# Performance work log

Hardware: AMD Instinct MI355X
Metric: run time of the kernel (lower is better)

The kernel has to match this reference:

```python
import jax, jax.numpy as jnp
import numpy as np

BS, TPD, D = 16384, 4, 128
G, M = 4, 4096


def setup_inputs() -> dict:
    key = jax.random.key(0)
    k1, k2 = jax.random.split(key)
    return {
        "x": jax.random.normal(k1, (BS, TPD, D), dtype=jnp.float32),
        "embeddings": jax.random.normal(k2, (G, M, D), dtype=jnp.float32),
        "count": jnp.zeros((G, M), dtype=jnp.float32),
    }


def reference(x, embeddings, count):
    bs, tpd, d = x.shape
    g, m, _ = embeddings.shape
    # (BS, TPD, D) -> (N, G, D) -> (G, N, D), N = BS*TPD/G
    xg = x.reshape(-1, g, d).transpose(1, 0, 2)
    # squared euclidean distances (argmin identical to cdist argmin)
    x2 = jnp.sum(xg * xg, axis=-1)[:, :, None]            # (G, N, 1)
    e2 = jnp.sum(embeddings * embeddings, axis=-1)[:, None, :]  # (G, 1, M)
    dist = x2 + e2 - 2.0 * jnp.einsum('gnd,gmd->gnm', xg, embeddings)  # (G, N, M)
    indices = jnp.argmin(dist, axis=-1)                   # (G, N) int
    # usage-count scatter add (buffer update in torch forward)
    new_count = count.at[jnp.arange(g)[:, None], indices].add(1.0)
    # gather quantized embeddings: (G, N, D)
    x_quant = embeddings[jnp.arange(g)[:, None], indices]
    x_quant = x_quant.transpose(1, 0, 2).reshape(bs, tpd, d)
    ind_out = indices.transpose(1, 0).reshape(bs, tpd)
    return (x_quant, ind_out, new_count)
```

## Files before the change

### kernel.cpp

```cpp
#include <hip/hip_runtime.h>

#define G 4
#define M 4096
#define D 128
#define NQ 16384
#define NROWS 65536
#define OFF_IND 8388608
#define OFF_CNT (OFF_IND + NROWS)
#define DELTA 0.02f

typedef unsigned int u32;
typedef unsigned short u16;
typedef __attribute__((ext_vector_type(8))) short bf16x8;
typedef __attribute__((ext_vector_type(4))) float f32x4;

__device__ __forceinline__ u16 f2bf(float f) {
    u32 u = __float_as_uint(f);
    return (u16)((u + 0x7FFFu + ((u >> 16) & 1u)) >> 16);
}
__device__ __forceinline__ float bf2f(u16 b) { return __uint_as_float((u32)b << 16); }

union bfpack { bf16x8 v; u32 u[4]; };


__global__ __launch_bounds__(256) void prep_emb_e2(const float* __restrict__ emb,
                                                   u32* __restrict__ efrag,
                                                   float* __restrict__ e2f) {
    const int tid = threadIdx.x, lane = tid & 63;
    const int c = blockIdx.x * 4 + (tid >> 6);
    const int ks = c & 3, mt = (c >> 2) & 255, g = c >> 10;
    const int m = mt * 16 + (lane & 15);
    const int k = ks * 32 + (lane >> 4) * 8;
    const float* src = emb + ((size_t)g * M + m) * D + k;
    const float4 a = *(const float4*)src;
    const float4 b = *(const float4*)(src + 4);
    const float v[8] = {a.x, a.y, a.z, a.w, b.x, b.y, b.z, b.w};
    float ss = 0.f;
#pragma unroll
    for (int i = 0; i < 8; ++i) ss = fmaf(v[i], v[i], ss);
    u32 hi[4], lo[4];
#pragma unroll
    for (int i = 0; i < 4; ++i) {
        const float v0 = v[2 * i], v1 = v[2 * i + 1];
        const u16 h0 = f2bf(v0), h1 = f2bf(v1);
        const u16 l0 = f2bf(v0 - bf2f(h0)), l1 = f2bf(v1 - bf2f(h1));
        hi[i] = (u32)h0 | ((u32)h1 << 16);
        lo[i] = (u32)l0 | ((u32)l1 << 16);
    }
    const u32 base = (u32)(g * 256 + mt) * 2048 + (u32)(ks * 2) * 256 + lane * 4;
    *(uint4*)(efrag + base)       = make_uint4(hi[0], hi[1], hi[2], hi[3]);
    *(uint4*)(efrag + base + 256) = make_uint4(lo[0], lo[1], lo[2], lo[3]);
    ss += __shfl_xor(ss, 16, 64);
    ss += __shfl_xor(ss, 32, 64);
    if (lane < 16) atomicAdd(&e2f[g * M + m], ss);
}

__global__ __launch_bounds__(256) void vq_mfma2(const float* __restrict__ x,
                                                const u32* __restrict__ efrag,
                                                const float* __restrict__ e2f,
                                                float* __restrict__ pb1,
                                                float* __restrict__ pb2,
                                                int* __restrict__ pi1) {
    __shared__ float e2s[2048];
    __shared__ u32 ebuf[2][2048];

    const int tid = threadIdx.x, w = tid >> 6, lane = tid & 63;
    const int combo = blockIdx.x & 7;
    const int g = combo >> 1, half = combo & 1;
    const int qb = blockIdx.x >> 3;

    const float* e2g = e2f + (size_t)g * M + half * 2048;
    for (int i = tid; i < 512; i += 256) ((float4*)e2s)[i] = ((const float4*)e2g)[i];

    const int qt0 = qb * 8 + w * 2;
    bf16x8 xf[2][4][2];
#pragma unroll
    for (int f = 0; f < 2; ++f) {
        const int n = (qt0 + f) * 16 + (lane & 15);
#pragma unroll
        for (int ks = 0; ks < 4; ++ks) {
            const int k = ks * 32 + (lane >> 4) * 8;
            const float* src = x + ((size_t)n * 4 + g) * D + k;
            const float4 a = *(const float4*)src;
            const float4 b = *(const float4*)(src + 4);
            const float v[8] = {a.x, a.y, a.z, a.w, b.x, b.y, b.z, b.w};
            bfpack ph, pl;
#pragma unroll
            for (int i = 0; i < 4; ++i) {
                const float v0 = -2.0f * v[2 * i], v1 = -2.0f * v[2 * i + 1];
                const u16 h0 = f2bf(v0), h1 = f2bf(v1);
                const u16 l0 = f2bf(v0 - bf2f(h0)), l1 = f2bf(v1 - bf2f(h1));
                ph.u[i] = (u32)h0 | ((u32)h1 << 16);
                pl.u[i] = (u32)l0 | ((u32)l1 << 16);
            }
            xf[f][ks][0] = ph.v;
            xf[f][ks][1] = pl.v;
        }
    }

    float b1[8], b2[8];
    int i1[8];
#pragma unroll
    for (int s = 0; s < 8; ++s) { b1[s] = 3.4e38f; b2[s] = 3.4e38f; i1[s] = 0; }

    const uint4* eg = (const uint4*)(efrag + (size_t)(g * 256 + half * 128) * 2048);
    {
        const uint4 s0 = eg[tid], s1 = eg[256 + tid];
        ((uint4*)ebuf[0])[tid] = s0;
        ((uint4*)ebuf[0])[256 + tid] = s1;
    }
    __syncthreads();

    int cur = 0;
    const int mb0 = half * 2048;
    for (int mc = 0; mc < 128; ++mc) {
        uint4 s0, s1;
        const bool pf = (mc + 1 < 128);
        if (pf) {
            const uint4* src = eg + (size_t)(mc + 1) * 512;
            s0 = src[tid];
            s1 = src[256 + tid];
        }
        const bf16x8* bp = (const bf16x8*)ebuf[cur];
        bf16x8 bh[4], bl[4];
#pragma unroll
        for (int ks = 0; ks < 4; ++ks) {
            bh[ks] = bp[(ks * 2 + 0) * 64 + lane];
            bl[ks] = bp[(ks * 2 + 1) * 64 + lane];
        }
        const int mcol = mb0 + mc * 16 + (lane & 15);
        const float e2c = e2s[mc * 16 + (lane & 15)];
        const f32x4 init = {e2c, e2c, e2c, e2c};
        f32x4 acc0, acc1;
        acc0 = __builtin_amdgcn_mfma_f32_16x16x32_bf16(xf[0][0][1], bh[0], init, 0, 0, 0);
        acc1 = __builtin_amdgcn_mfma_f32_16x16x32_bf16(xf[1][0][1], bh[0], init, 0, 0, 0);
#pragma unroll
        for (int ks = 1; ks < 4; ++ks) {
            acc0 = __builtin_amdgcn_mfma_f32_16x16x32_bf16(xf[0][ks][1], bh[ks], acc0, 0, 0, 0);
            acc1 = __builtin_amdgcn_mfma_f32_16x16x32_bf16(xf[1][ks][1], bh[ks], acc1, 0, 0, 0);
        }
#pragma unroll
        for (int ks = 0; ks < 4; ++ks) {
            acc0 = __builtin_amdgcn_mfma_f32_16x16x32_bf16(xf[0][ks][0], bl[ks], acc0, 0, 0, 0);
            acc1 = __builtin_amdgcn_mfma_f32_16x16x32_bf16(xf[1][ks][0], bl[ks], acc1, 0, 0, 0);
        }
#pragma unroll
        for (int ks = 0; ks < 4; ++ks) {
            acc0 = __builtin_amdgcn_mfma_f32_16x16x32_bf16(xf[0][ks][0], bh[ks], acc0, 0, 0, 0);
            acc1 = __builtin_amdgcn_mfma_f32_16x16x32_bf16(xf[1][ks][0], bh[ks], acc1, 0, 0, 0);
        }
#pragma unroll
        for (int r = 0; r < 4; ++r) {
            const float s0v = acc0[r];
            b2[r] = fminf(b2[r], fmaxf(b1[r], s0v));
            i1[r] = (s0v < b1[r]) ? mcol : i1[r];
            b1[r] = fminf(b1[r], s0v);
            const float s1v = acc1[r];
            b2[r + 4] = fminf(b2[r + 4], fmaxf(b1[r + 4], s1v));
            i1[r + 4] = (s1v < b1[r + 4]) ? mcol : i1[r + 4];
            b1[r + 4] = fminf(b1[r + 4], s1v);
        }
        if (pf) {
            uint4* dst = (uint4*)ebuf[cur ^ 1];
            dst[tid] = s0;
            dst[256 + tid] = s1;
        }
        __syncthreads();
        cur ^= 1;
    }

#pragma unroll
    for (int s = 0; s < 8; ++s) {
        float v1 = b1[s], v2 = b2[s];
        int j1 = i1[s];
#pragma unroll
        for (int off = 1; off < 16; off <<= 1) {
            const float o1 = __shfl_xor(v1, off, 64);
            const int   oj = __shfl_xor(j1, off, 64);
            const float o2 = __shfl_xor(v2, off, 64);
            v2 = fminf(fminf(v2, o2), fmaxf(v1, o1));
            if (o1 < v1 || (o1 == v1 && oj < j1)) { v1 = o1; j1 = oj; }
        }
        if ((lane & 15) == 0) {
            const int n = (qt0 + (s >> 2)) * 16 + (lane >> 4) * 4 + (s & 3);
            const int pidx = ((((g << 14) | n)) << 1) | half;
            pb1[pidx] = v1;
            pb2[pidx] = v2;
            pi1[pidx] = j1;
        }
    }
}

__global__ __launch_bounds__(256) void merge_kernel(const float* __restrict__ pb1,
                                                    const float* __restrict__ pb2,
                                                    const int* __restrict__ pi1,
                                                    float* __restrict__ out,
                                                    int* __restrict__ flagcnt,
                                                    int* __restrict__ flaglist) {
    const int t = blockIdx.x * 256 + threadIdx.x;
    const float v1a = pb1[2 * t], v1b = pb1[2 * t + 1];
    const float v2a = pb2[2 * t], v2b = pb2[2 * t + 1];
    const int   ia = pi1[2 * t],  ib = pi1[2 * t + 1];
    const float v1 = fminf(v1a, v1b);
    const int   i  = (v1b < v1a) ? ib : ia;
    const float v2 = fminf(fminf(v2a, v2b), fmaxf(v1a, v1b));
    const int g = t >> 14, n = t & 16383;
    if (v2 - v1 > DELTA) {
        out[(size_t)OFF_IND + (size_t)n * 4 + g] = (float)i;
        atomicAdd(out + OFF_CNT + (size_t)g * M + i, 1.0f);
    } else {
        const int pos = atomicAdd(flagcnt, 1);
        flaglist[pos] = t;
    }
}

__global__ __launch_bounds__(256) void recheck(const float* __restrict__ x,
                                               const float* __restrict__ emb,
                                               const int* __restrict__ flagcnt,
                                               const int* __restrict__ flaglist,
                                               float* __restrict__ out) {
    __shared__ float xs[D];
    __shared__ double wv[4];
    __shared__ int wi[4];
    const int tid = threadIdx.x;
    int nf = *flagcnt;
    if (nf > NROWS) nf = NROWS;
    for (int it = blockIdx.x; it < nf; it += gridDim.x) {
        const int qid = flaglist[it];
        const int g = qid >> 14, n = qid & 16383;
        __syncthreads();
        if (tid < 32) ((float4*)xs)[tid] = ((const float4*)(x + ((size_t)n * 4 + g) * D))[tid];
        __syncthreads();
        double best = 1e300;
        int bi = 0;
        for (int j = 0; j < 16; ++j) {
            const int m = tid + j * 256;
            const float* e = emb + ((size_t)g * M + m) * D;
            double dot = 0.0, ee = 0.0;
            for (int k = 0; k < D; k += 4) {
                const float4 ev = *(const float4*)(e + k);
                const double e0 = ev.x, e1 = ev.y, e2v = ev.z, e3 = ev.w;
                dot = fma((double)xs[k + 0], e0, dot);
                dot = fma((double)xs[k + 1], e1, dot);
                dot = fma((double)xs[k + 2], e2v, dot);
                dot = fma((double)xs[k + 3], e3, dot);
                ee = fma(e0, e0, ee); ee = fma(e1, e1, ee);
                ee = fma(e2v, e2v, ee); ee = fma(e3, e3, ee);
            }
            const double s = ee - 2.0 * dot;
            if (s < best) { best = s; bi = m; }
        }
        for (int off = 1; off < 64; off <<= 1) {
            const double ob = __shfl_xor(best, off, 64);
            const int oi = __shfl_xor(bi, off, 64);
            if (ob < best || (ob == best && oi < bi)) { best = ob; bi = oi; }
        }
        if ((tid & 63) == 0) { wv[tid >> 6] = best; wi[tid >> 6] = bi; }
        __syncthreads();
        if (tid == 0) {
            double bv = wv[0];
            int bj = wi[0];
            for (int u = 1; u < 4; ++u)
                if (wv[u] < bv || (wv[u] == bv && wi[u] < bj)) { bv = wv[u]; bj = wi[u]; }
            out[(size_t)OFF_IND + (size_t)n * 4 + g] = (float)bj;
            atomicAdd(out + OFF_CNT + (size_t)g * M + bj, 1.0f);
        }
    }
}

__global__ __launch_bounds__(256) void gather_kernel(const float* __restrict__ emb,
                                                     const float* __restrict__ indf,
                                                     float* __restrict__ xq) {
    const int rid = blockIdx.x * 8 + (threadIdx.x >> 5);
    const int lane = threadIdx.x & 31;
    const int g = rid & 3;
    const int m = (int)indf[rid];
    const float4 v = ((const float4*)(emb + ((size_t)g * M + m) * D))[lane];
    ((float4*)(xq + (size_t)rid * D))[lane] = v;
}


#define QT 64
#define MT 128
#define KT 32
#define XPAD 132
#define EPAD 36

__global__ __launch_bounds__(256) void e2d_kernel(const float* __restrict__ emb,
                                                  double* __restrict__ e2) {
    int row = blockIdx.x * 4 + (threadIdx.x >> 6);
    int lane = threadIdx.x & 63;
    const float2 v = ((const float2*)(emb + (size_t)row * D))[lane];
    double s = (double)v.x * (double)v.x + (double)v.y * (double)v.y;
#pragma unroll
    for (int off = 1; off < 64; off <<= 1) s += __shfl_xor(s, off, 64);
    if (lane == 0) e2[row] = s;
}

__global__ __launch_bounds__(256) void argmin_kernel(const float* __restrict__ x,
                                                     const float* __restrict__ emb,
                                                     const double* __restrict__ e2,
                                                     float* __restrict__ out) {
    __shared__ float xs[QT][XPAD];
    __shared__ float es[MT][EPAD];
    const int g = blockIdx.x >> 8;
    const int n0 = (blockIdx.x & 255) * QT;
    const int tid = threadIdx.x;
    const int tm = tid & 15;
    const int tq = tid >> 4;
#pragma unroll
    for (int it = 0; it < 8; ++it) {
        int idx = it * 256 + tid;
        int r = idx >> 5, c2 = idx & 31;
        const float4 v = ((const float4*)(x + ((size_t)((n0 + r) * 4 + g)) * D))[c2];
        *(float4*)&xs[r][c2 * 4] = v;
    }
    double best[4];
    int bm[4];
#pragma unroll
    for (int qi = 0; qi < 4; ++qi) { best[qi] = 1e300; bm[qi] = 0; }
    const double* e2g = e2 + (size_t)g * M;
    const float* eg = emb + (size_t)g * M * D;
    for (int mc = 0; mc < M / MT; ++mc) {
        const int m0 = mc * MT;
        double acc[4][8];
#pragma unroll
        for (int qi = 0; qi < 4; ++qi)
#pragma unroll
            for (int mi = 0; mi < 8; ++mi) acc[qi][mi] = 0.0;
        for (int kc = 0; kc < D / KT; ++kc) {
            __syncthreads();
#pragma unroll
            for (int it = 0; it < 4; ++it) {
                int idx = it * 256 + tid;
                int r = idx >> 3, c2 = idx & 7;
                const float4 v = ((const float4*)(eg + (size_t)(m0 + r) * D + kc * KT))[c2];
                *(float4*)&es[r][c2 * 4] = v;
            }
            __syncthreads();
#pragma unroll
            for (int kk = 0; kk < KT; kk += 4) {
                double xv[4][4];
#pragma unroll
                for (int qi = 0; qi < 4; ++qi) {
                    const float4 v = *(const float4*)&xs[tq + 16 * qi][kc * KT + kk];
                    xv[qi][0] = v.x; xv[qi][1] = v.y; xv[qi][2] = v.z; xv[qi][3] = v.w;
                }
#pragma unroll
                for (int mi = 0; mi < 8; ++mi) {
                    const float4 v = *(const float4*)&es[tm + 16 * mi][kk];
                    const double e0 = v.x, e1 = v.y, e2v = v.z, e3 = v.w;
#pragma unroll
                    for (int qi = 0; qi < 4; ++qi) {
                        acc[qi][mi] = fma(xv[qi][0], e0, acc[qi][mi]);
                        acc[qi][mi] = fma(xv[qi][1], e1, acc[qi][mi]);
                        acc[qi][mi] = fma(xv[qi][2], e2v, acc[qi][mi]);
                        acc[qi][mi] = fma(xv[qi][3], e3, acc[qi][mi]);
                    }
                }
            }
        }
#pragma unroll
        for (int mi = 0; mi < 8; ++mi) {
            const int m = m0 + tm + 16 * mi;
            const double e2m = e2g[m];
#pragma unroll
            for (int qi = 0; qi < 4; ++qi) {
                const double s = e2m - 2.0 * acc[qi][mi];
                if (s < best[qi]) { best[qi] = s; bm[qi] = m; }
            }
        }
    }
#pragma unroll
    for (int qi = 0; qi < 4; ++qi) {
        double v = best[qi];
        int i = bm[qi];
#pragma unroll
        for (int off = 1; off < 16; off <<= 1) {
            const double ov = __shfl_xor(v, off, 64);
            const int oi = __shfl_xor(i, off, 64);
            if (ov < v || (ov == v && oi < i)) { v = ov; i = oi; }
        }
        if (tm == 0) {
            const int n = n0 + tq + 16 * qi;
            out[(size_t)OFF_IND + (size_t)n * 4 + g] = (float)i;
            atomicAdd(out + OFF_CNT + (size_t)g * M + i, 1.0f);
        }
    }
}


extern "C" void kernel_launch(void* const* d_in, const int* in_sizes, int n_in,
                              void* d_out, int out_size, void* d_ws, size_t ws_size,
                              hipStream_t stream) {
    const float* x   = (const float*)d_in[0];
    const float* emb = (const float*)d_in[1];
    const float* cnt = (const float*)d_in[2];
    float* out = (float*)d_out;

    if (ws_size >= 8716544) {
        u32*   efrag    = (u32*)d_ws;
        float* e2fp     = (float*)((char*)d_ws + 8388608);
        int*   flagcnt  = (int*)((char*)d_ws + 8454144);
        int*   flaglist = (int*)((char*)d_ws + 8454400);
        float* pb1 = out;
        float* pb2 = out + 131072;
        int*   pi1 = (int*)(out + 262144);

        hipMemsetAsync((char*)d_ws + 8388608, 0, 65792, stream);
        hipLaunchKernelGGL(prep_emb_e2, dim3(1024), dim3(256), 0, stream, emb, efrag, e2fp);
        hipMemcpyAsync(out + OFF_CNT, cnt, (size_t)G * M * sizeof(float),
                       hipMemcpyDeviceToDevice, stream);
        hipLaunchKernelGGL(vq_mfma2, dim3(1024), dim3(256), 0, stream,
                           x, efrag, e2fp, pb1, pb2, pi1);
        hipLaunchKernelGGL(merge_kernel, dim3(256), dim3(256), 0, stream,
                           pb1, pb2, pi1, out, flagcnt, flaglist);
        hipLaunchKernelGGL(recheck, dim3(2048), dim3(256), 0, stream,
                           x, emb, flagcnt, flaglist, out);
        hipLaunchKernelGGL(gather_kernel, dim3(NROWS / 8), dim3(256), 0, stream,
                           emb, out + OFF_IND, out);
    } else {
        double* e2 = (double*)d_ws;
        hipLaunchKernelGGL(e2d_kernel, dim3(4096), dim3(256), 0, stream, emb, e2);
        hipMemcpyAsync(out + OFF_CNT, cnt, (size_t)G * M * sizeof(float),
                       hipMemcpyDeviceToDevice, stream);
        hipLaunchKernelGGL(argmin_kernel, dim3((NQ / QT) * G), dim3(256), 0, stream,
                           x, emb, e2, out);
        hipLaunchKernelGGL(gather_kernel, dim3(NROWS / 8), dim3(256), 0, stream,
                           emb, out + OFF_IND, out);
    }
}
```

Baseline: 356.7 us.

## Switch distance GEMM to 32x32x16 MFMA tiles with precomputed embedding norms

The main argmin kernel now uses 32x32x16 bf16 MFMA with a 32-wide tile per wave, and the embedding fragment layout and double-buffered LDS chunk size change to match. Embedding squared norms are computed in double by a separate kernel instead of by atomics, which also removes a memset. The recheck kernel reuses these precomputed double norms instead of recomputing them per candidate. It also adds s_setprio around the MFMA block, med3 for the second-best tracking, and launch bounds for 3 blocks per CU. Each wave's tile of 32 queries times 32 codes is meant to raise MFMA efficiency and reuse of fragments loaded from LDS, at the cost of more registers and a doubled LDS buffer.

```diff
diff --git a/kernel.cpp b/kernel.cpp
--- a/kernel.cpp
+++ b/kernel.cpp
@@ -13,6 +13,7 @@
 typedef unsigned short u16;
 typedef __attribute__((ext_vector_type(8))) short bf16x8;
 typedef __attribute__((ext_vector_type(4))) float f32x4;
+typedef __attribute__((ext_vector_type(16))) float f32x16;
 
 __device__ __forceinline__ u16 f2bf(float f) {
     u32 u = __float_as_uint(f);
@@ -23,46 +24,57 @@
 union bfpack { bf16x8 v; u32 u[4]; };
 
 
-__global__ __launch_bounds__(256) void prep_emb_e2(const float* __restrict__ emb,
-                                                   u32* __restrict__ efrag,
-                                                   float* __restrict__ e2f) {
-    const int tid = threadIdx.x, lane = tid & 63;
-    const int c = blockIdx.x * 4 + (tid >> 6);
-    const int ks = c & 3, mt = (c >> 2) & 255, g = c >> 10;
-    const int m = mt * 16 + (lane & 15);
-    const int k = ks * 32 + (lane >> 4) * 8;
-    const float* src = emb + ((size_t)g * M + m) * D + k;
-    const float4 a = *(const float4*)src;
-    const float4 b = *(const float4*)(src + 4);
-    const float v[8] = {a.x, a.y, a.z, a.w, b.x, b.y, b.z, b.w};
-    float ss = 0.f;
-#pragma unroll
-    for (int i = 0; i < 8; ++i) ss = fmaf(v[i], v[i], ss);
-    u32 hi[4], lo[4];
-#pragma unroll
-    for (int i = 0; i < 4; ++i) {
-        const float v0 = v[2 * i], v1 = v[2 * i + 1];
-        const u16 h0 = f2bf(v0), h1 = f2bf(v1);
-        const u16 l0 = f2bf(v0 - bf2f(h0)), l1 = f2bf(v1 - bf2f(h1));
-        hi[i] = (u32)h0 | ((u32)h1 << 16);
-        lo[i] = (u32)l0 | ((u32)l1 << 16);
-    }
-    const u32 base = (u32)(g * 256 + mt) * 2048 + (u32)(ks * 2) * 256 + lane * 4;
-    *(uint4*)(efrag + base)       = make_uint4(hi[0], hi[1], hi[2], hi[3]);
-    *(uint4*)(efrag + base + 256) = make_uint4(lo[0], lo[1], lo[2], lo[3]);
-    ss += __shfl_xor(ss, 16, 64);
-    ss += __shfl_xor(ss, 32, 64);
-    if (lane < 16) atomicAdd(&e2f[g * M + m], ss);
-}
-
-__global__ __launch_bounds__(256) void vq_mfma2(const float* __restrict__ x,
-                                                const u32* __restrict__ efrag,
-                                                const float* __restrict__ e2f,
-                                                float* __restrict__ pb1,
-                                                float* __restrict__ pb2,
-                                                int* __restrict__ pi1) {
+__global__ __launch_bounds__(256) void e2both(const float* __restrict__ emb,
+                                              float* __restrict__ e2f,
+                                              double* __restrict__ e2d,
+                                              int* __restrict__ flagcnt) {
+    const int row = blockIdx.x * 4 + (threadIdx.x >> 6);
+    const int lane = threadIdx.x & 63;
+    const float2 v = ((const float2*)(emb + (size_t)row * D))[lane];
+    double s = (double)v.x * (double)v.x + (double)v.y * (double)v.y;
+#pragma unroll
+    for (int off = 1; off < 64; off <<= 1) s += __shfl_xor(s, off, 64);
+    if (lane == 0) { e2f[row] = (float)s; e2d[row] = s; }
+    if (blockIdx.x == 0 && threadIdx.x == 0) *flagcnt = 0;
+}
+
+__global__ __launch_bounds__(256) void prep_emb(const float* __restrict__ emb,
+                                                u32* __restrict__ efrag) {
+    const int tid = threadIdx.x;
+    const int g = blockIdx.x >> 7, mt = blockIdx.x & 127;
+    u32* chunk = efrag + (size_t)(g * 128 + mt) * 4096;
+#pragma unroll
+    for (int rep = 0; rep < 2; ++rep) {
+        const int idx = rep * 256 + tid;
+        const int kk = idx >> 6, lane = idx & 63;
+        const int m = mt * 32 + (lane & 31);
+        const int k = kk * 16 + (lane >> 5) * 8;
+        const float* src = emb + ((size_t)g * M + m) * D + k;
+        const float4 a = *(const float4*)src;
+        const float4 b = *(const float4*)(src + 4);
+        const float v[8] = {a.x, a.y, a.z, a.w, b.x, b.y, b.z, b.w};
+        u32 hi[4], lo[4];
+#pragma unroll
+        for (int i = 0; i < 4; ++i) {
+            const float v0 = v[2 * i], v1 = v[2 * i + 1];
+            const u16 h0 = f2bf(v0), h1 = f2bf(v1);
+            const u16 l0 = f2bf(v0 - bf2f(h0)), l1 = f2bf(v1 - bf2f(h1));
+            hi[i] = (u32)h0 | ((u32)h1 << 16);
+            lo[i] = (u32)l0 | ((u32)l1 << 16);
+        }
+        *(uint4*)(chunk + (size_t)((kk * 2 + 0) * 64 + lane) * 4) = make_uint4(hi[0], hi[1], hi[2], hi[3]);
+        *(uint4*)(chunk + (size_t)((kk * 2 + 1) * 64 + lane) * 4) = make_uint4(lo[0], lo[1], lo[2], lo[3]);
+    }
+}
+
+__global__ __launch_bounds__(256, 3) void vq_mfma3(const float* __restrict__ x,
+                                                   const u32* __restrict__ efrag,
+                                                   const float* __restrict__ e2f,
+                                                   float* __restrict__ pb1,
+                                                   float* __restrict__ pb2,
+                                                   int* __restrict__ pi1) {
     __shared__ float e2s[2048];
-    __shared__ u32 ebuf[2][2048];
+    __shared__ u32 ebuf[2][4096];
 
     const int tid = threadIdx.x, w = tid >> 6, lane = tid & 63;
     const int combo = blockIdx.x & 7;
@@ -72,118 +84,93 @@
     const float* e2g = e2f + (size_t)g * M + half * 2048;
     for (int i = tid; i < 512; i += 256) ((float4*)e2s)[i] = ((const float4*)e2g)[i];
 
-    const int qt0 = qb * 8 + w * 2;
-    bf16x8 xf[2][4][2];
-#pragma unroll
-    for (int f = 0; f < 2; ++f) {
-        const int n = (qt0 + f) * 16 + (lane & 15);
-#pragma unroll
-        for (int ks = 0; ks < 4; ++ks) {
-            const int k = ks * 32 + (lane >> 4) * 8;
-            const float* src = x + ((size_t)n * 4 + g) * D + k;
-            const float4 a = *(const float4*)src;
-            const float4 b = *(const float4*)(src + 4);
-            const float v[8] = {a.x, a.y, a.z, a.w, b.x, b.y, b.z, b.w};
-            bfpack ph, pl;
-#pragma unroll
-            for (int i = 0; i < 4; ++i) {
-                const float v0 = -2.0f * v[2 * i], v1 = -2.0f * v[2 * i + 1];
-                const u16 h0 = f2bf(v0), h1 = f2bf(v1);
-                const u16 l0 = f2bf(v0 - bf2f(h0)), l1 = f2bf(v1 - bf2f(h1));
-                ph.u[i] = (u32)h0 | ((u32)h1 << 16);
-                pl.u[i] = (u32)l0 | ((u32)l1 << 16);
-            }
-            xf[f][ks][0] = ph.v;
-            xf[f][ks][1] = pl.v;
-        }
-    }
-
-    float b1[8], b2[8];
-    int i1[8];
-#pragma unroll
-    for (int s = 0; s < 8; ++s) { b1[s] = 3.4e38f; b2[s] = 3.4e38f; i1[s] = 0; }
-
-    const uint4* eg = (const uint4*)(efrag + (size_t)(g * 256 + half * 128) * 2048);
+    const int qrow = qb * 128 + w * 32 + (lane & 31);
+    bf16x8 xh[8], xl[8];
+#pragma unroll
+    for (int kk = 0; kk < 8; ++kk) {
+        const int k = kk * 16 + (lane >> 5) * 8;
+        const float* src = x + ((size_t)qrow * 4 + g) * D + k;
+        const float4 a = *(const float4*)src;
+        const float4 b = *(const float4*)(src + 4);
+        const float v[8] = {a.x, a.y, a.z, a.w, b.x, b.y, b.z, b.w};
+        bfpack ph, pl;
+#pragma unroll
+        for (int i = 0; i < 4; ++i) {
+            const float v0 = -2.0f * v[2 * i], v1 = -2.0f * v[2 * i + 1];
+            const u16 h0 = f2bf(v0), h1 = f2bf(v1);
+            const u16 l0 = f2bf(v0 - bf2f(h0)), l1 = f2bf(v1 - bf2f(h1));
+            ph.u[i] = (u32)h0 | ((u32)h1 << 16);
+            pl.u[i] = (u32)l0 | ((u32)l1 << 16);
+        }
+        xh[kk] = ph.v;
+        xl[kk] = pl.v;
+    }
+
+    float b1[16], b2[16];
+    int i1[16];
+#pragma unroll
+    for (int r = 0; r < 16; ++r) { b1[r] = 3.4e38f; b2[r] = 3.4e38f; i1[r] = 0; }
+
+    const uint4* eg = (const uint4*)(efrag + (size_t)(g * 128 + half * 64) * 4096);
     {
-        const uint4 s0 = eg[tid], s1 = eg[256 + tid];
-        ((uint4*)ebuf[0])[tid] = s0;
-        ((uint4*)ebuf[0])[256 + tid] = s1;
+        const uint4 t0 = eg[tid], t1 = eg[256 + tid], t2 = eg[512 + tid], t3 = eg[768 + tid];
+        uint4* db = (uint4*)ebuf[0];
+        db[tid] = t0; db[256 + tid] = t1; db[512 + tid] = t2; db[768 + tid] = t3;
     }
     __syncthreads();
 
-    int cur = 0;
-    const int mb0 = half * 2048;
-    for (int mc = 0; mc < 128; ++mc) {
-        uint4 s0, s1;
-        const bool pf = (mc + 1 < 128);
-        if (pf) {
-            const uint4* src = eg + (size_t)(mc + 1) * 512;
-            s0 = src[tid];
-            s1 = src[256 + tid];
+    for (int t = 0; t < 64; ++t) {
+        const int cur = t & 1;
+        uint4 s0, s1, s2, s3;
+        if (t < 63) {
+            const uint4* src = eg + (size_t)(t + 1) * 1024;
+            s0 = src[tid]; s1 = src[256 + tid]; s2 = src[512 + tid]; s3 = src[768 + tid];
         }
         const bf16x8* bp = (const bf16x8*)ebuf[cur];
-        bf16x8 bh[4], bl[4];
-#pragma unroll
-        for (int ks = 0; ks < 4; ++ks) {
-            bh[ks] = bp[(ks * 2 + 0) * 64 + lane];
-            bl[ks] = bp[(ks * 2 + 1) * 64 + lane];
-        }
-        const int mcol = mb0 + mc * 16 + (lane & 15);
-        const float e2c = e2s[mc * 16 + (lane & 15)];
-        const f32x4 init = {e2c, e2c, e2c, e2c};
-        f32x4 acc0, acc1;
-        acc0 = __builtin_amdgcn_mfma_f32_16x16x32_bf16(xf[0][0][1], bh[0], init, 0, 0, 0);
-        acc1 = __builtin_amdgcn_mfma_f32_16x16x32_bf16(xf[1][0][1], bh[0], init, 0, 0, 0);
-#pragma unroll
-        for (int ks = 1; ks < 4; ++ks) {
-            acc0 = __builtin_amdgcn_mfma_f32_16x16x32_bf16(xf[0][ks][1], bh[ks], acc0, 0, 0, 0);
-            acc1 = __builtin_amdgcn_mfma_f32_16x16x32_bf16(xf[1][ks][1], bh[ks], acc1, 0, 0, 0);
-        }
-#pragma unroll
-        for (int ks = 0; ks < 4; ++ks) {
-            acc0 = __builtin_amdgcn_mfma_f32_16x16x32_bf16(xf[0][ks][0], bl[ks], acc0, 0, 0, 0);
-            acc1 = __builtin_amdgcn_mfma_f32_16x16x32_bf16(xf[1][ks][0], bl[ks], acc1, 0, 0, 0);
-        }
-#pragma unroll
-        for (int ks = 0; ks < 4; ++ks) {
-            acc0 = __builtin_amdgcn_mfma_f32_16x16x32_bf16(xf[0][ks][0], bh[ks], acc0, 0, 0, 0);
-            acc1 = __builtin_amdgcn_mfma_f32_16x16x32_bf16(xf[1][ks][0], bh[ks], acc1, 0, 0, 0);
-        }
-#pragma unroll
-        for (int r = 0; r < 4; ++r) {
-            const float s0v = acc0[r];
-            b2[r] = fminf(b2[r], fmaxf(b1[r], s0v));
-            i1[r] = (s0v < b1[r]) ? mcol : i1[r];
-            b1[r] = fminf(b1[r], s0v);
-            const float s1v = acc1[r];
-            b2[r + 4] = fminf(b2[r + 4], fmaxf(b1[r + 4], s1v));
-            i1[r + 4] = (s1v < b1[r + 4]) ? mcol : i1[r + 4];
-            b1[r + 4] = fminf(b1[r + 4], s1v);
-        }
-        if (pf) {
-            uint4* dst = (uint4*)ebuf[cur ^ 1];
-            dst[tid] = s0;
-            dst[256 + tid] = s1;
+        const float e2c = e2s[t * 32 + (lane & 31)];
+        f32x16 acc;
+#pragma unroll
+        for (int r = 0; r < 16; ++r) acc[r] = e2c;
+        __builtin_amdgcn_s_setprio(1);
+#pragma unroll
+        for (int kk = 0; kk < 8; ++kk) {
+            const bf16x8 bh = bp[(kk * 2 + 0) * 64 + lane];
+            const bf16x8 bl = bp[(kk * 2 + 1) * 64 + lane];
+            acc = __builtin_amdgcn_mfma_f32_32x32x16_bf16(xl[kk], bh, acc, 0, 0, 0);
+            acc = __builtin_amdgcn_mfma_f32_32x32x16_bf16(xh[kk], bl, acc, 0, 0, 0);
+            acc = __builtin_amdgcn_mfma_f32_32x32x16_bf16(xh[kk], bh, acc, 0, 0, 0);
+        }
+        __builtin_amdgcn_s_setprio(0);
+        const int mcol = half * 2048 + t * 32 + (lane & 31);
+#pragma unroll
+        for (int r = 0; r < 16; ++r) {
+            const float s = acc[r];
+            b2[r] = __builtin_amdgcn_fmed3f(s, b1[r], b2[r]);
+            i1[r] = (s < b1[r]) ? mcol : i1[r];
+            b1[r] = fminf(b1[r], s);
+        }
+        if (t < 63) {
+            uint4* db = (uint4*)ebuf[cur ^ 1];
+            db[tid] = s0; db[256 + tid] = s1; db[512 + tid] = s2; db[768 + tid] = s3;
         }
         __syncthreads();
-        cur ^= 1;
-    }
-
-#pragma unroll
-    for (int s = 0; s < 8; ++s) {
-        float v1 = b1[s], v2 = b2[s];
-        int j1 = i1[s];
-#pragma unroll
-        for (int off = 1; off < 16; off <<= 1) {
+    }
+
+#pragma unroll
+    for (int r = 0; r < 16; ++r) {
+        float v1 = b1[r], v2 = b2[r];
+        int j1 = i1[r];
+#pragma unroll
+        for (int off = 1; off < 32; off <<= 1) {
             const float o1 = __shfl_xor(v1, off, 64);
             const int   oj = __shfl_xor(j1, off, 64);
             const float o2 = __shfl_xor(v2, off, 64);
             v2 = fminf(fminf(v2, o2), fmaxf(v1, o1));
             if (o1 < v1 || (o1 == v1 && oj < j1)) { v1 = o1; j1 = oj; }
         }
-        if ((lane & 15) == 0) {
-            const int n = (qt0 + (s >> 2)) * 16 + (lane >> 4) * 4 + (s & 3);
-            const int pidx = ((((g << 14) | n)) << 1) | half;
+        if ((lane & 31) == 0) {
+            const int q = qb * 128 + w * 32 + (r & 3) + 8 * (r >> 2) + 4 * (lane >> 5);
+            const int pidx = ((((g << 14) | q)) << 1) | half;
             pb1[pidx] = v1;
             pb2[pidx] = v2;
             pi1[pidx] = j1;
@@ -216,6 +203,7 @@
 
 __global__ __launch_bounds__(256) void recheck(const float* __restrict__ x,
                                                const float* __restrict__ emb,
+                                               const double* __restrict__ e2d,
                                                const int* __restrict__ flagcnt,
                                                const int* __restrict__ flaglist,
                                                float* __restrict__ out) {
@@ -236,18 +224,15 @@
         for (int j = 0; j < 16; ++j) {
             const int m = tid + j * 256;
             const float* e = emb + ((size_t)g * M + m) * D;
-            double dot = 0.0, ee = 0.0;
+            double dot = 0.0;
             for (int k = 0; k < D; k += 4) {
                 const float4 ev = *(const float4*)(e + k);
-                const double e0 = ev.x, e1 = ev.y, e2v = ev.z, e3 = ev.w;
-                dot = fma((double)xs[k + 0], e0, dot);
-                dot = fma((double)xs[k + 1], e1, dot);
-                dot = fma((double)xs[k + 2], e2v, dot);
-                dot = fma((double)xs[k + 3], e3, dot);
-                ee = fma(e0, e0, ee); ee = fma(e1, e1, ee);
-                ee = fma(e2v, e2v, ee); ee = fma(e3, e3, ee);
+                dot = fma((double)xs[k + 0], (double)ev.x, dot);
+                dot = fma((double)xs[k + 1], (double)ev.y, dot);
+                dot = fma((double)xs[k + 2], (double)ev.z, dot);
+                dot = fma((double)xs[k + 3], (double)ev.w, dot);
             }
-            const double s = ee - 2.0 * dot;
+            const double s = e2d[(size_t)g * M + m] - 2.0 * dot;
             if (s < best) { best = s; bi = m; }
         }
         for (int off = 1; off < 64; off <<= 1) {
@@ -398,25 +383,26 @@
     const float* cnt = (const float*)d_in[2];
     float* out = (float*)d_out;
 
-    if (ws_size >= 8716544) {
-        u32*   efrag    = (u32*)d_ws;
-        float* e2fp     = (float*)((char*)d_ws + 8388608);
-        int*   flagcnt  = (int*)((char*)d_ws + 8454144);
-        int*   flaglist = (int*)((char*)d_ws + 8454400);
-        float* pb1 = out;
-        float* pb2 = out + 131072;
-        int*   pi1 = (int*)(out + 262144);
-
-        hipMemsetAsync((char*)d_ws + 8388608, 0, 65792, stream);
-        hipLaunchKernelGGL(prep_emb_e2, dim3(1024), dim3(256), 0, stream, emb, efrag, e2fp);
+    if (ws_size >= 8454148) {
+        u32*    efrag   = (u32*)d_ws;
+        float*  e2fp    = (float*)((char*)d_ws + 8388608);
+        int*    flagcnt = (int*)((char*)d_ws + 8454144);
+        float*  pb1      = out;
+        float*  pb2      = out + 131072;
+        int*    pi1      = (int*)(out + 262144);
+        int*    flaglist = (int*)(out + 393216);
+        double* e2d      = (double*)(out + 458752);
+
+        hipLaunchKernelGGL(e2both, dim3(4096), dim3(256), 0, stream, emb, e2fp, e2d, flagcnt);
+        hipLaunchKernelGGL(prep_emb, dim3(512), dim3(256), 0, stream, emb, efrag);
         hipMemcpyAsync(out + OFF_CNT, cnt, (size_t)G * M * sizeof(float),
                        hipMemcpyDeviceToDevice, stream);
-        hipLaunchKernelGGL(vq_mfma2, dim3(1024), dim3(256), 0, stream,
+        hipLaunchKernelGGL(vq_mfma3, dim3(1024), dim3(256), 0, stream,
                            x, efrag, e2fp, pb1, pb2, pi1);
         hipLaunchKernelGGL(merge_kernel, dim3(256), dim3(256), 0, stream,
                            pb1, pb2, pi1, out, flagcnt, flaglist);
         hipLaunchKernelGGL(recheck, dim3(2048), dim3(256), 0, stream,
-                           x, emb, flagcnt, flaglist, out);
+                           x, emb, e2d, flagcnt, flaglist, out);
         hipLaunchKernelGGL(gather_kernel, dim3(NROWS / 8), dim3(256), 0, stream,
                            emb, out + OFF_IND, out);
     } else {
```

Result: slower. 375.2 us (+5.2%).
